# Kernel tuning notes

Measured on AMD Instinct MI355X. Metric: run time of the kernel, lower is better.

The kernel has to match this reference:

```python
import jax, jax.numpy as jnp
import numpy as np

_EPS = 1e-5
RC = 5.0   # cutoff radius
L = 20     # number of radial basis functions
N = 10000  # nodes
E = 100000 # edges
F = 128    # in_feats


def _ssp(x):
    # ShiftedSoftplus: softplus(x) - log(2)
    return jax.nn.softplus(x) - jnp.log(2.0)


def _rbf(r):
    # DimeNet radial basis: sqrt(2/rc) * sin(n*pi*r/rc) / r, n = 1..L.  r: [E,1] -> [E,L]
    n = jnp.arange(1, L + 1, dtype=r.dtype)
    return jnp.sqrt(2.0 / RC) * jnp.sin(n * jnp.pi * r / RC) / r


def _fc(u):
    # cosine cutoff applied elementwise: 0.5*(cos(pi*u/rc)+1) for u < rc else 0
    return jnp.where(u < RC, 0.5 * (jnp.cos(jnp.pi * u / RC) + 1.0), 0.0)


def setup_inputs() -> dict:
    key = jax.random.key(0)
    ks = jax.random.split(key, 12)

    def nrm(k, shape, scale=1.0):
        return jax.random.normal(k, shape, dtype=jnp.float32) * scale

    return {
        "x": nrm(ks[0], (N, 3)) * 3.0,           # atomic positions
        "v": nrm(ks[1], (N, F, 3)),               # vector node features
        "s": nrm(ks[2], (N, F)),                  # scalar node features
        "ms1_w": nrm(ks[3], (F, F), F ** -0.5),
        "ms1_b": jnp.zeros((F,), jnp.float32),
        "ms2_w": nrm(ks[4], (3 * F, F), F ** -0.5),
        "ms2_b": jnp.zeros((3 * F,), jnp.float32),
        "mv_w": nrm(ks[5], (3 * F, L), L ** -0.5),
        "mv_b": jnp.zeros((3 * F,), jnp.float32),
        "us1_w": nrm(ks[6], (F, F), F ** -0.5),
        "us1_b": jnp.zeros((F,), jnp.float32),
        "us2_w": nrm(ks[7], (3 * F, F), F ** -0.5),
        "us2_b": jnp.zeros((3 * F,), jnp.float32),
        "src": jax.random.randint(ks[8], (E,), 0, N, dtype=jnp.int32),
        "dst": jax.random.randint(ks[9], (E,), 0, N, dtype=jnp.int32),
    }


def reference(x, v, s, ms1_w, ms1_b, ms2_w, ms2_b, mv_w, mv_b,
              us1_w, us1_b, us2_w, us2_b, src, dst):
    # ---------- pass 1: message1 + reduce1 (sum over incoming edges) ----------
    sj = s[src]                                   # [E,F]   src scalar features
    vj = v[src]                                   # [E,F,3] src vector features
    vec = x[src] - x[dst]                         # [E,3]   x_i - x_j (molecule branch)
    r = jnp.sqrt(jnp.sum(vec ** 2, axis=-1) + _EPS)[:, None]          # [E,1]
    phi = _ssp(sj @ ms1_w.T + ms1_b) @ ms2_w.T + ms2_b                 # [E,3F]
    w = _fc(_rbf(r) @ mv_w.T + mv_b)                                    # [E,3F]
    v_, s_, r_ = jnp.split(phi * w, 3, axis=-1)                         # each [E,F]
    dv_e = vj * v_[:, :, None] + r_[:, :, None] * (vec / r)[:, None, :] # [E,F,3]
    dv = jax.ops.segment_sum(dv_e, dst, num_segments=N)                 # [N,F,3]
    ds = jax.ops.segment_sum(s_, dst, num_segments=N)                   # [N,F]
    v_new = v + dv
    s_new = s + ds

    # ---------- pass 2: message2 + reduce2 (mean over incoming edges) ----------
    s2 = _ssp(s_new[src] @ us1_w.T + us1_b) @ us2_w.T + us2_b           # [E,3F]
    deg = jax.ops.segment_sum(jnp.ones((E,), s.dtype), dst, num_segments=N)
    denom = jnp.maximum(deg, 1.0)
    s_mean = jax.ops.segment_sum(s2, dst, num_segments=N) / denom[:, None]        # [N,3F]
    uv = jax.ops.segment_sum(v_new[src], dst, num_segments=N) / denom[:, None, None]  # [N,F,3]
    avv, asv, ass = jnp.split(s_mean, 3, axis=-1)                       # each [N,F]
    norm = jnp.sqrt(jnp.sum(uv ** 2, axis=-1) + _EPS)[..., None]        # [N,F,1]
    dv2 = uv * avv[:, :, None]                                           # [N,F,3]
    ds2 = jnp.sum((uv / norm) ** 2, axis=-1) * asv + ass                 # [N,F]
    return (v_new + dv2, s_new + ds2)
```

## Files before the change

### kernel.cpp

```cpp
#include <hip/hip_runtime.h>
#include <hip/hip_bf16.h>


#define F_DIM   128
#define F3_DIM  384
#define L_DIM   20
#define CAP     64
#define BATCH   16

typedef __attribute__((ext_vector_type(8))) short short8;
typedef __attribute__((ext_vector_type(4))) float f32x4;
typedef __attribute__((ext_vector_type(4))) unsigned short us4;

struct u3 { unsigned a, b, c; };

__device__ __forceinline__ unsigned short f2bf(float f) {
  union { float f; unsigned u; } a; a.f = f;
  unsigned u = a.u;
  u = (u + 0x7FFFu + ((u >> 16) & 1u)) >> 16;
  return (unsigned short)u;
}
__device__ __forceinline__ float bf2f(unsigned short u) {
  union { unsigned u; float f; } a; a.u = ((unsigned)u) << 16;
  return a.f;
}

__global__ __launch_bounds__(256) void cast_fill_kernel(
    const float* __restrict__ ms1_w, unsigned short* __restrict__ w_ms1,
    const float* __restrict__ ms2_w, unsigned short* __restrict__ w_ms2,
    const float* __restrict__ us1_w, unsigned short* __restrict__ w_us1,
    const float* __restrict__ us2_w, unsigned short* __restrict__ w_us2,
    const float* __restrict__ s,     unsigned short* __restrict__ sbf,
    const float* __restrict__ v,     us4* __restrict__ v4,
    const float* __restrict__ mv_w,  unsigned short* __restrict__ mvwB,
    const int* __restrict__ src, const int* __restrict__ dst,
    int* __restrict__ cursor, int* __restrict__ jbuf,
    unsigned short* __restrict__ c1pad, unsigned short* __restrict__ v4pad,
    int nF, int E)
{
  int i = blockIdx.x * 256 + threadIdx.x;
  if (i < 16384) w_ms1[i] = f2bf(ms1_w[i]);
  if (i < 49152) w_ms2[i] = f2bf(ms2_w[i]);
  if (i < 16384) w_us1[i] = f2bf(us1_w[i]);
  if (i < 49152) w_us2[i] = f2bf(us2_w[i]);
  if (i < nF)    sbf[i] = f2bf(s[i]);
  if (i < nF) {
    const float* vp = v + (size_t)i * 3;
    us4 o; o.x = f2bf(vp[0]); o.y = f2bf(vp[1]); o.z = f2bf(vp[2]); o.w = 0;
    v4[i] = o;
  }
  if (i < 384 * 32) {
    int o = i >> 5, k = i & 31;
    float val = (k < 20) ? mv_w[o * 20 + k] * 0.6324555320336759f : 0.f;
    mvwB[i] = f2bf(val);
  }
  if (i < 768) c1pad[i] = 0;
  if (i < 512) v4pad[i] = 0;
  if (i < E) {
    int d = dst[i];
    int p = atomicAdd(&cursor[d], 1);
    if (p < CAP) jbuf[d * CAP + p] = src[i];
  }
}

__global__ __launch_bounds__(512) void mlp_kernel(
    const unsigned short* __restrict__ X,
    const unsigned short* __restrict__ W1,
    const float* __restrict__ B1,
    const unsigned short* __restrict__ W2,
    const float* __restrict__ B2,
    const us4* __restrict__ Vin,
    unsigned short* __restrict__ Yc)
{
  __shared__ float HT[128 * 17];
  const int lane = threadIdx.x & 63;
  const int wave = threadIdx.x >> 6;
  const int c    = lane & 15;
  const int quad = lane >> 4;
  const int m0   = blockIdx.x * 16;

  f32x4 acc = (f32x4){0.f, 0.f, 0.f, 0.f};
#pragma unroll
  for (int kk = 0; kk < 4; kk++) {
    short8 a = *(const short8*)(X + (size_t)(m0 + c) * 128 + kk * 32 + quad * 8);
    short8 b = *(const short8*)(W1 + (size_t)(wave * 16 + c) * 128 + kk * 32 + quad * 8);
    acc = __builtin_amdgcn_mfma_f32_16x16x32_bf16(a, b, acc, 0, 0, 0);
  }
  {
    int k = wave * 16 + c;
    float bias = B1[k];
#pragma unroll
    for (int r = 0; r < 4; r++) {
      float h = acc[r] + bias;
      float sp = (h > 15.f) ? h : log1pf(__expf(h));
      sp -= 0.69314718056f;
      HT[k * 17 + quad * 4 + r] = sp;
    }
  }
  __syncthreads();

  f32x4 acc2[3];
#pragma unroll
  for (int g = 0; g < 3; g++) acc2[g] = (f32x4){0.f, 0.f, 0.f, 0.f};
#pragma unroll
  for (int kk = 0; kk < 4; kk++) {
    short8 afr;
#pragma unroll
    for (int j = 0; j < 8; j++) {
      float hv = HT[(kk * 32 + quad * 8 + j) * 17 + c];
      afr[j] = (short)f2bf(hv);
    }
#pragma unroll
    for (int g = 0; g < 3; g++) {
      short8 b = *(const short8*)(W2 + (size_t)(g * 128 + wave * 16 + c) * 128 + kk * 32 + quad * 8);
      acc2[g] = __builtin_amdgcn_mfma_f32_16x16x32_bf16(afr, b, acc2[g], 0, 0, 0);
    }
  }
  {
    int f = wave * 16 + c;
    float b0 = B2[f], b1 = B2[128 + f], b2 = B2[256 + f];
#pragma unroll
    for (int r = 0; r < 4; r++) {
      int m = quad * 4 + r;
      us4 vv = Vin[(size_t)(m0 + m) * 128 + f];
      unsigned p0 = f2bf(acc2[0][r] + b0);
      unsigned p1 = f2bf(acc2[1][r] + b1);
      unsigned p2 = f2bf(acc2[2][r] + b2);
      u3 rec;
      rec.a = p0 | (p1 << 16);
      rec.b = p2 | ((unsigned)vv.x << 16);
      rec.c = (unsigned)vv.y | ((unsigned)vv.z << 16);
      *(u3*)(Yc + ((size_t)(m0 + m) * 128 + f) * 6) = rec;
    }
  }
}

__global__ __launch_bounds__(512) void hidden_kernel(
    const unsigned short* __restrict__ X,
    const unsigned short* __restrict__ W1,
    const float* __restrict__ B1,
    us4* __restrict__ V4)
{
  const int lane = threadIdx.x & 63;
  const int wave = threadIdx.x >> 6;
  const int c    = lane & 15;
  const int quad = lane >> 4;
  const int m0   = blockIdx.x * 16;

  f32x4 acc = (f32x4){0.f, 0.f, 0.f, 0.f};
#pragma unroll
  for (int kk = 0; kk < 4; kk++) {
    short8 a = *(const short8*)(X + (size_t)(m0 + c) * 128 + kk * 32 + quad * 8);
    short8 b = *(const short8*)(W1 + (size_t)(wave * 16 + c) * 128 + kk * 32 + quad * 8);
    acc = __builtin_amdgcn_mfma_f32_16x16x32_bf16(a, b, acc, 0, 0, 0);
  }
  int f = wave * 16 + c;
  float bias = B1[f];
#pragma unroll
  for (int r = 0; r < 4; r++) {
    int m = m0 + quad * 4 + r;
    float h = acc[r] + bias;
    float sp = (h > 15.f) ? h : log1pf(__expf(h));
    sp -= 0.69314718056f;
    us4 rec = V4[(size_t)m * 128 + f];
    rec.w = f2bf(sp);
    V4[(size_t)m * 128 + f] = rec;
  }
}

__global__ __launch_bounds__(256, 4) void pass1_kernel(
    const float* __restrict__ x,
    const unsigned short* __restrict__ combo1,
    const float* __restrict__ v,
    const float* __restrict__ s,
    const unsigned short* __restrict__ mvwB,
    const float* __restrict__ mv_b,
    const int* __restrict__ jbuf,
    const int* __restrict__ deg,
    float* __restrict__ vnew, us4* __restrict__ vnew4,
    float* __restrict__ snew, unsigned short* __restrict__ snew_bf, int nNodes)
{
  __shared__ unsigned short Asn[BATCH * 32];
  __shared__ float4 Au[BATCH];
  __shared__ us4 Wl[BATCH * 128];
  __shared__ float red[512];

  const int tid  = threadIdx.x;
  const int wave = tid >> 6, lane = tid & 63;
  const int half = wave >> 1, split = wave & 1;
  const int i = blockIdx.x;
  const int f = lane + 64 * half;
  const int c = lane & 15, quad = lane >> 4;

  int cnt = deg[i]; if (cnt > CAP) cnt = CAP;
  const int base = i * CAP;

  short8 bfr[6]; float bias[6];
#pragma unroll
  for (int p = 0; p < 3; p++)
#pragma unroll
    for (int h = 0; h < 2; h++) {
      int t = 2 * wave + h + 8 * p;
      bfr[p * 2 + h]  = *(const short8*)(mvwB + (size_t)(t * 16 + c) * 32 + quad * 8);
      bias[p * 2 + h] = mv_b[t * 16 + c];
    }

  const float xi0 = x[i * 3], xi1 = x[i * 3 + 1], xi2 = x[i * 3 + 2];
  int jv = (lane < cnt) ? jbuf[base + lane] : nNodes;

  float accV0 = 0.f, accV1 = 0.f, accV2 = 0.f, accS = 0.f;

  for (int bs = 0; bs < cnt; bs += BATCH) {
    int bcnt = cnt - bs; if (bcnt > BATCH) bcnt = BATCH;
    __syncthreads();

    if (wave == 0) {
      int t16 = lane & (BATCH - 1);
      int e = bs + t16;
      int j = __shfl(jv, e);
      if (lane < BATCH && e < cnt) {
        float d0 = x[j * 3]     - xi0;
        float d1 = x[j * 3 + 1] - xi1;
        float d2 = x[j * 3 + 2] - xi2;
        float r = sqrtf(d0 * d0 + d1 * d1 + d2 * d2 + 1e-5f);
        float invr = 1.0f / r;
        Au[lane] = make_float4(d0 * invr, d1 * invr, d2 * invr, invr);
        float theta = r * 0.6283185307179586f;
        float s1, c1;
        __sincosf(theta, &s1, &c1);
        float c2 = 2.f * c1;
        float pm2 = s1, pm1 = c2 * s1;
        Asn[lane * 32 + 0] = f2bf(pm2);
        Asn[lane * 32 + 1] = f2bf(pm1);
#pragma unroll
        for (int l = 2; l < L_DIM; l++) {
          float cur = c2 * pm1 - pm2;
          Asn[lane * 32 + l] = f2bf(cur);
          pm2 = pm1; pm1 = cur;
        }
#pragma unroll
        for (int l = L_DIM; l < 32; l++) Asn[lane * 32 + l] = 0;
      }
    }
    __syncthreads();

    {
      short8 a = *(const short8*)&Asn[c * 32 + quad * 8];
      f32x4 acc[6];
#pragma unroll
      for (int q = 0; q < 6; q++)
        acc[q] = __builtin_amdgcn_mfma_f32_16x16x32_bf16(
            a, bfr[q], (f32x4){0.f, 0.f, 0.f, 0.f}, 0, 0, 0);
#pragma unroll
      for (int r = 0; r < 4; r++) {
        int el = quad * 4 + r;
        if (el < bcnt) {
          float invr = Au[el].w;
#pragma unroll
          for (int h = 0; h < 2; h++) {
            float wp0 = fmaf(acc[h][r],     invr, bias[h]);
            float wp1 = fmaf(acc[2 + h][r], invr, bias[2 + h]);
            float wp2 = fmaf(acc[4 + h][r], invr, bias[4 + h]);
            float w0 = (wp0 < 5.f) ? 0.5f * (__cosf(wp0 * 0.6283185307179586f) + 1.f) : 0.f;
            float w1 = (wp1 < 5.f) ? 0.5f * (__cosf(wp1 * 0.6283185307179586f) + 1.f) : 0.f;
            float w2 = (wp2 < 5.f) ? 0.5f * (__cosf(wp2 * 0.6283185307179586f) + 1.f) : 0.f;
            us4 o; o.x = f2bf(w0); o.y = f2bf(w1); o.z = f2bf(w2); o.w = 0;
            Wl[el * 128 + wave * 32 + h * 16 + c] = o;
          }
        }
      }
    }
    __syncthreads();

    u3 cb[8];
#pragma unroll
    for (int k = 0; k < 8; k++) {
      int j = __shfl(jv, bs + split + 2 * k);
      cb[k] = *(const u3*)(combo1 + ((size_t)j * 128 + f) * 6);
    }
#pragma unroll
    for (int k = 0; k < 8; k++) {
      int el = split + 2 * k;
      if (el < bcnt) {
        float4 u = Au[el];
        us4 wv = Wl[el * 128 + f];
        float ph0 = bf2f((unsigned short)(cb[k].a & 0xffff));
        float ph1 = bf2f((unsigned short)(cb[k].a >> 16));
        float ph2 = bf2f((unsigned short)(cb[k].b & 0xffff));
        float vx  = bf2f((unsigned short)(cb[k].b >> 16));
        float vy  = bf2f((unsigned short)(cb[k].c & 0xffff));
        float vz  = bf2f((unsigned short)(cb[k].c >> 16));
        float m0 = ph0 * bf2f(wv.x);
        float m1 = ph1 * bf2f(wv.y);
        float m2 = ph2 * bf2f(wv.z);
        accV0 = fmaf(vx, m0, fmaf(m2, u.x, accV0));
        accV1 = fmaf(vy, m0, fmaf(m2, u.y, accV1));
        accV2 = fmaf(vz, m0, fmaf(m2, u.z, accV2));
        accS += m1;
      }
    }
  }

  const int idx = half * 64 + lane;
  __syncthreads();
  if (split == 1) {
    red[idx * 4 + 0] = accV0; red[idx * 4 + 1] = accV1;
    red[idx * 4 + 2] = accV2; red[idx * 4 + 3] = accS;
  }
  __syncthreads();
  if (split == 0) {
    accV0 += red[idx * 4 + 0]; accV1 += red[idx * 4 + 1];
    accV2 += red[idx * 4 + 2]; accS  += red[idx * 4 + 3];
    size_t b3 = (size_t)i * 384 + f * 3;
    float n0 = v[b3] + accV0, n1 = v[b3 + 1] + accV1, n2 = v[b3 + 2] + accV2;
    vnew[b3] = n0; vnew[b3 + 1] = n1; vnew[b3 + 2] = n2;
    us4 o; o.x = f2bf(n0); o.y = f2bf(n1); o.z = f2bf(n2); o.w = 0;
    vnew4[(size_t)i * 128 + f] = o;
    size_t b1 = (size_t)i * 128 + f;
    float sv = s[b1] + accS;
    snew[b1] = sv;
    snew_bf[b1] = f2bf(sv);
  }
}

__global__ __launch_bounds__(512, 2) void pass2_kernel(
    const us4* __restrict__ vnew4,
    const int* __restrict__ jbuf, const int* __restrict__ deg,
    const unsigned short* __restrict__ W2,
    const float* __restrict__ B2,
    const float* __restrict__ vnew,
    const float* __restrict__ snew,
    float* __restrict__ vout, float* __restrict__ sout, int nNodes)
{
  __shared__ unsigned short HMb[16][136];
  __shared__ float UV[16 * 128 * 3];

  const int tid  = threadIdx.x;
  const int wave = tid >> 6, lane = tid & 63;
  const int c    = lane & 15, quad = lane >> 4;
  const int m0   = blockIdx.x * 16;

  const int ra = 2 * wave, rb = ra + 1;
  const int na = m0 + ra, nb = m0 + rb;
  int ca = deg[na]; if (ca > CAP) ca = CAP;
  int cb = deg[nb]; if (cb > CAP) cb = CAP;
  int jva = (lane < ca) ? jbuf[na * CAP + lane] : nNodes;
  int jvb = (lane < cb) ? jbuf[nb * CAP + lane] : nNodes;

  float a0l = 0.f, a1l = 0.f, a2l = 0.f, ahl = 0.f;
  float a0h = 0.f, a1h = 0.f, a2h = 0.f, ahh = 0.f;
  float b0l = 0.f, b1l = 0.f, b2l = 0.f, bhl = 0.f;
  float b0h = 0.f, b1h = 0.f, b2h = 0.f, bhh = 0.f;

  int emax = (ca > cb) ? ca : cb;
  for (int e = 0; e < emax; ++e) {
    int ja = __shfl(jva, e);
    int jb = __shfl(jvb, e);
    us4 ral = vnew4[(size_t)ja * 128 + lane];
    us4 rah = vnew4[(size_t)ja * 128 + lane + 64];
    us4 rbl = vnew4[(size_t)jb * 128 + lane];
    us4 rbh = vnew4[(size_t)jb * 128 + lane + 64];
    a0l += bf2f(ral.x); a1l += bf2f(ral.y); a2l += bf2f(ral.z); ahl += bf2f(ral.w);
    a0h += bf2f(rah.x); a1h += bf2f(rah.y); a2h += bf2f(rah.z); ahh += bf2f(rah.w);
    b0l += bf2f(rbl.x); b1l += bf2f(rbl.y); b2l += bf2f(rbl.z); bhl += bf2f(rbl.w);
    b0h += bf2f(rbh.x); b1h += bf2f(rbh.y); b2h += bf2f(rbh.z); bhh += bf2f(rbh.w);
  }

  float dia = 1.0f / (float)(ca > 0 ? ca : 1);
  float dib = 1.0f / (float)(cb > 0 ? cb : 1);
  {
    int fl = lane, fh = lane + 64;
    UV[(ra * 128 + fl) * 3 + 0] = a0l * dia;
    UV[(ra * 128 + fl) * 3 + 1] = a1l * dia;
    UV[(ra * 128 + fl) * 3 + 2] = a2l * dia;
    UV[(ra * 128 + fh) * 3 + 0] = a0h * dia;
    UV[(ra * 128 + fh) * 3 + 1] = a1h * dia;
    UV[(ra * 128 + fh) * 3 + 2] = a2h * dia;
    UV[(rb * 128 + fl) * 3 + 0] = b0l * dib;
    UV[(rb * 128 + fl) * 3 + 1] = b1l * dib;
    UV[(rb * 128 + fl) * 3 + 2] = b2l * dib;
    UV[(rb * 128 + fh) * 3 + 0] = b0h * dib;
    UV[(rb * 128 + fh) * 3 + 1] = b1h * dib;
    UV[(rb * 128 + fh) * 3 + 2] = b2h * dib;
    HMb[ra][fl] = f2bf(ahl * dia);
    HMb[ra][fh] = f2bf(ahh * dia);
    HMb[rb][fl] = f2bf(bhl * dib);
    HMb[rb][fh] = f2bf(bhh * dib);
  }
  __syncthreads();

  f32x4 acc2[3];
#pragma unroll
  for (int g = 0; g < 3; g++) acc2[g] = (f32x4){0.f, 0.f, 0.f, 0.f};
#pragma unroll
  for (int kk = 0; kk < 4; kk++) {
    short8 afr = *(const short8*)&HMb[c][kk * 32 + quad * 8];
#pragma unroll
    for (int g = 0; g < 3; g++) {
      short8 b = *(const short8*)(W2 + (size_t)(g * 128 + wave * 16 + c) * 128 + kk * 32 + quad * 8);
      acc2[g] = __builtin_amdgcn_mfma_f32_16x16x32_bf16(afr, b, acc2[g], 0, 0, 0);
    }
  }

  int f = wave * 16 + c;
  float bb0 = B2[f], bb1 = B2[128 + f], bb2 = B2[256 + f];
#pragma unroll
  for (int r = 0; r < 4; r++) {
    int m = quad * 4 + r;
    int gm = m0 + m;
    float z = (deg[gm] > 0) ? 1.f : 0.f;
    float avv = (acc2[0][r] + bb0) * z;
    float asv = (acc2[1][r] + bb1) * z;
    float ass = (acc2[2][r] + bb2) * z;
    float uv0 = UV[(m * 128 + f) * 3 + 0];
    float uv1 = UV[(m * 128 + f) * 3 + 1];
    float uv2 = UV[(m * 128 + f) * 3 + 2];
    float q = uv0 * uv0 + uv1 * uv1 + uv2 * uv2;
    float ds2 = (q / (q + 1e-5f)) * asv + ass;
    size_t b3 = (size_t)gm * 384 + f * 3;
    vout[b3]     = vnew[b3]     + uv0 * avv;
    vout[b3 + 1] = vnew[b3 + 1] + uv1 * avv;
    vout[b3 + 2] = vnew[b3 + 2] + uv2 * avv;
    size_t b1i = (size_t)gm * 128 + f;
    sout[b1i] = snew[b1i] + ds2;
  }
}

extern "C" void kernel_launch(void* const* d_in, const int* in_sizes, int n_in,
                              void* d_out, int out_size, void* d_ws, size_t ws_size,
                              hipStream_t stream)
{
  const float* x     = (const float*)d_in[0];
  const float* v     = (const float*)d_in[1];
  const float* s     = (const float*)d_in[2];
  const float* ms1_w = (const float*)d_in[3];
  const float* ms1_b = (const float*)d_in[4];
  const float* ms2_w = (const float*)d_in[5];
  const float* ms2_b = (const float*)d_in[6];
  const float* mv_w  = (const float*)d_in[7];
  const float* mv_b  = (const float*)d_in[8];
  const float* us1_w = (const float*)d_in[9];
  const float* us1_b = (const float*)d_in[10];
  const float* us2_w = (const float*)d_in[11];
  const float* us2_b = (const float*)d_in[12];
  const int*   src   = (const int*)d_in[13];
  const int*   dst   = (const int*)d_in[14];

  const int N = in_sizes[0] / 3;
  const int E = in_sizes[13];

  char* p = (char*)d_ws;
  auto alloc = [&](size_t bytes) -> void* {
    void* r = (void*)p;
    p += (bytes + 255) & ~(size_t)255;
    return r;
  };
  unsigned short* sbf   = (unsigned short*)alloc((size_t)N * 128 * 2);
  unsigned short* snbf  = (unsigned short*)alloc((size_t)N * 128 * 2);
  unsigned short* w_ms1 = (unsigned short*)alloc(16384 * 2);
  unsigned short* w_ms2 = (unsigned short*)alloc(49152 * 2);
  unsigned short* w_us1 = (unsigned short*)alloc(16384 * 2);
  unsigned short* w_us2 = (unsigned short*)alloc(49152 * 2);
  unsigned short* mvwB  = (unsigned short*)alloc(384 * 32 * 2);
  us4*   v4     = (us4*)alloc((size_t)N * 128 * 8);
  us4*   vnew4  = (us4*)alloc((size_t)(N + 1) * 128 * 8);
  unsigned short* combo1 = (unsigned short*)alloc((size_t)(N + 1) * 128 * 12);
  float* vnew   = (float*)alloc((size_t)N * 384 * 4);
  float* snew   = (float*)alloc((size_t)N * 128 * 4);
  int* cursor   = (int*)alloc((size_t)N * 4);
  int* jbuf     = (int*)alloc((size_t)N * CAP * 4);

  hipMemsetAsync(cursor, 0, (size_t)N * 4, stream);

  cast_fill_kernel<<<(N * 128 + 255) / 256, 256, 0, stream>>>(
      ms1_w, w_ms1, ms2_w, w_ms2, us1_w, w_us1, us2_w, w_us2,
      s, sbf, v, v4, mv_w, mvwB, src, dst, cursor, jbuf,
      combo1 + (size_t)N * 768, (unsigned short*)(vnew4 + (size_t)N * 128),
      N * 128, E);

  mlp_kernel<<<N / 16, 512, 0, stream>>>(sbf, w_ms1, ms1_b, w_ms2, ms2_b,
                                         v4, combo1);

  pass1_kernel<<<N, 256, 0, stream>>>(x, combo1, v, s, mvwB, mv_b,
                                      jbuf, cursor, vnew, vnew4, snew, snbf, N);

  hidden_kernel<<<N / 16, 512, 0, stream>>>(snbf, w_us1, us1_b, vnew4);

  float* vout = (float*)d_out;
  float* sout = vout + (size_t)N * 384;
  pass2_kernel<<<N / 16, 512, 0, stream>>>(vnew4, jbuf, cursor, w_us2, us2_b,
                                           vnew, snew, vout, sout, N);
}
```

Baseline: 213.3 us.

## Fuse v bf16 cast into MLP, parallelize RBF setup, unroll pass2 gather

The bf16 conversion of v moves out of cast_fill_kernel into the MLP epilogue, which now reads fp32 v directly, so the intermediate v4 buffer and its write and re-read are gone. In pass1 the radial-basis setup is spread across all threads (16 threads per edge), each computing sin(n*theta) directly instead of one wave running a serial Chebyshev recurrence per edge. The pass2 gather loop is unrolled by two edges to keep more loads in flight. The costs are more transcendental calls per edge and a strided fp32 read of v in the MLP epilogue.

```diff
diff --git a/kernel.cpp b/kernel.cpp
--- a/kernel.cpp
+++ b/kernel.cpp
@@ -31,7 +31,6 @@
     const float* __restrict__ us1_w, unsigned short* __restrict__ w_us1,
     const float* __restrict__ us2_w, unsigned short* __restrict__ w_us2,
     const float* __restrict__ s,     unsigned short* __restrict__ sbf,
-    const float* __restrict__ v,     us4* __restrict__ v4,
     const float* __restrict__ mv_w,  unsigned short* __restrict__ mvwB,
     const int* __restrict__ src, const int* __restrict__ dst,
     int* __restrict__ cursor, int* __restrict__ jbuf,
@@ -44,11 +43,6 @@
   if (i < 16384) w_us1[i] = f2bf(us1_w[i]);
   if (i < 49152) w_us2[i] = f2bf(us2_w[i]);
   if (i < nF)    sbf[i] = f2bf(s[i]);
-  if (i < nF) {
-    const float* vp = v + (size_t)i * 3;
-    us4 o; o.x = f2bf(vp[0]); o.y = f2bf(vp[1]); o.z = f2bf(vp[2]); o.w = 0;
-    v4[i] = o;
-  }
   if (i < 384 * 32) {
     int o = i >> 5, k = i & 31;
     float val = (k < 20) ? mv_w[o * 20 + k] * 0.6324555320336759f : 0.f;
@@ -69,7 +63,7 @@
     const float* __restrict__ B1,
     const unsigned short* __restrict__ W2,
     const float* __restrict__ B2,
-    const us4* __restrict__ Vin,
+    const float* __restrict__ Vfp,
     unsigned short* __restrict__ Yc)
 {
   __shared__ float HT[128 * 17];
@@ -122,14 +116,14 @@
 #pragma unroll
     for (int r = 0; r < 4; r++) {
       int m = quad * 4 + r;
-      us4 vv = Vin[(size_t)(m0 + m) * 128 + f];
+      const float* vp = Vfp + ((size_t)(m0 + m) * 128 + f) * 3;
       unsigned p0 = f2bf(acc2[0][r] + b0);
       unsigned p1 = f2bf(acc2[1][r] + b1);
       unsigned p2 = f2bf(acc2[2][r] + b2);
       u3 rec;
       rec.a = p0 | (p1 << 16);
-      rec.b = p2 | ((unsigned)vv.x << 16);
-      rec.c = (unsigned)vv.y | ((unsigned)vv.z << 16);
+      rec.b = p2 | ((unsigned)f2bf(vp[0]) << 16);
+      rec.c = (unsigned)f2bf(vp[1]) | ((unsigned)f2bf(vp[2]) << 16);
       *(u3*)(Yc + ((size_t)(m0 + m) * 128 + f) * 6) = rec;
     }
   }
@@ -214,32 +208,22 @@
     int bcnt = cnt - bs; if (bcnt > BATCH) bcnt = BATCH;
     __syncthreads();
 
-    if (wave == 0) {
-      int t16 = lane & (BATCH - 1);
-      int e = bs + t16;
-      int j = __shfl(jv, e);
-      if (lane < BATCH && e < cnt) {
+    {
+      int e  = tid >> 4;
+      int li = tid & 15;
+      int j  = __shfl(jv, bs + e);
+      if (e < bcnt) {
         float d0 = x[j * 3]     - xi0;
         float d1 = x[j * 3 + 1] - xi1;
         float d2 = x[j * 3 + 2] - xi2;
         float r = sqrtf(d0 * d0 + d1 * d1 + d2 * d2 + 1e-5f);
         float invr = 1.0f / r;
-        Au[lane] = make_float4(d0 * invr, d1 * invr, d2 * invr, invr);
+        if (li == 0) Au[e] = make_float4(d0 * invr, d1 * invr, d2 * invr, invr);
         float theta = r * 0.6283185307179586f;
-        float s1, c1;
-        __sincosf(theta, &s1, &c1);
-        float c2 = 2.f * c1;
-        float pm2 = s1, pm1 = c2 * s1;
-        Asn[lane * 32 + 0] = f2bf(pm2);
-        Asn[lane * 32 + 1] = f2bf(pm1);
-#pragma unroll
-        for (int l = 2; l < L_DIM; l++) {
-          float cur = c2 * pm1 - pm2;
-          Asn[lane * 32 + l] = f2bf(cur);
-          pm2 = pm1; pm1 = cur;
-        }
-#pragma unroll
-        for (int l = L_DIM; l < 32; l++) Asn[lane * 32 + l] = 0;
+        Asn[e * 32 + li] = f2bf(__sinf((float)(li + 1) * theta));
+        unsigned short hiv = 0;
+        if (li < 4) hiv = f2bf(__sinf((float)(li + 17) * theta));
+        Asn[e * 32 + 16 + li] = hiv;
       }
     }
     __syncthreads();
@@ -353,17 +337,27 @@
   float b0h = 0.f, b1h = 0.f, b2h = 0.f, bhh = 0.f;
 
   int emax = (ca > cb) ? ca : cb;
-  for (int e = 0; e < emax; ++e) {
-    int ja = __shfl(jva, e);
-    int jb = __shfl(jvb, e);
-    us4 ral = vnew4[(size_t)ja * 128 + lane];
-    us4 rah = vnew4[(size_t)ja * 128 + lane + 64];
-    us4 rbl = vnew4[(size_t)jb * 128 + lane];
-    us4 rbh = vnew4[(size_t)jb * 128 + lane + 64];
-    a0l += bf2f(ral.x); a1l += bf2f(ral.y); a2l += bf2f(ral.z); ahl += bf2f(ral.w);
-    a0h += bf2f(rah.x); a1h += bf2f(rah.y); a2h += bf2f(rah.z); ahh += bf2f(rah.w);
-    b0l += bf2f(rbl.x); b1l += bf2f(rbl.y); b2l += bf2f(rbl.z); bhl += bf2f(rbl.w);
-    b0h += bf2f(rbh.x); b1h += bf2f(rbh.y); b2h += bf2f(rbh.z); bhh += bf2f(rbh.w);
+  for (int e = 0; e < emax; e += 2) {
+    int ja0 = __shfl(jva, e);
+    int jb0 = __shfl(jvb, e);
+    int ja1 = __shfl(jva, e + 1);
+    int jb1 = __shfl(jvb, e + 1);
+    us4 r0al = vnew4[(size_t)ja0 * 128 + lane];
+    us4 r0ah = vnew4[(size_t)ja0 * 128 + lane + 64];
+    us4 r0bl = vnew4[(size_t)jb0 * 128 + lane];
+    us4 r0bh = vnew4[(size_t)jb0 * 128 + lane + 64];
+    us4 r1al = vnew4[(size_t)ja1 * 128 + lane];
+    us4 r1ah = vnew4[(size_t)ja1 * 128 + lane + 64];
+    us4 r1bl = vnew4[(size_t)jb1 * 128 + lane];
+    us4 r1bh = vnew4[(size_t)jb1 * 128 + lane + 64];
+    a0l += bf2f(r0al.x) + bf2f(r1al.x); a1l += bf2f(r0al.y) + bf2f(r1al.y);
+    a2l += bf2f(r0al.z) + bf2f(r1al.z); ahl += bf2f(r0al.w) + bf2f(r1al.w);
+    a0h += bf2f(r0ah.x) + bf2f(r1ah.x); a1h += bf2f(r0ah.y) + bf2f(r1ah.y);
+    a2h += bf2f(r0ah.z) + bf2f(r1ah.z); ahh += bf2f(r0ah.w) + bf2f(r1ah.w);
+    b0l += bf2f(r0bl.x) + bf2f(r1bl.x); b1l += bf2f(r0bl.y) + bf2f(r1bl.y);
+    b2l += bf2f(r0bl.z) + bf2f(r1bl.z); bhl += bf2f(r0bl.w) + bf2f(r1bl.w);
+    b0h += bf2f(r0bh.x) + bf2f(r1bh.x); b1h += bf2f(r0bh.y) + bf2f(r1bh.y);
+    b2h += bf2f(r0bh.z) + bf2f(r1bh.z); bhh += bf2f(r0bh.w) + bf2f(r1bh.w);
   }
 
   float dia = 1.0f / (float)(ca > 0 ? ca : 1);
@@ -462,7 +456,6 @@
   unsigned short* w_us1 = (unsigned short*)alloc(16384 * 2);
   unsigned short* w_us2 = (unsigned short*)alloc(49152 * 2);
   unsigned short* mvwB  = (unsigned short*)alloc(384 * 32 * 2);
-  us4*   v4     = (us4*)alloc((size_t)N * 128 * 8);
   us4*   vnew4  = (us4*)alloc((size_t)(N + 1) * 128 * 8);
   unsigned short* combo1 = (unsigned short*)alloc((size_t)(N + 1) * 128 * 12);
   float* vnew   = (float*)alloc((size_t)N * 384 * 4);
@@ -474,12 +467,12 @@
 
   cast_fill_kernel<<<(N * 128 + 255) / 256, 256, 0, stream>>>(
       ms1_w, w_ms1, ms2_w, w_ms2, us1_w, w_us1, us2_w, w_us2,
-      s, sbf, v, v4, mv_w, mvwB, src, dst, cursor, jbuf,
+      s, sbf, mv_w, mvwB, src, dst, cursor, jbuf,
       combo1 + (size_t)N * 768, (unsigned short*)(vnew4 + (size_t)N * 128),
       N * 128, E);
 
   mlp_kernel<<<N / 16, 512, 0, stream>>>(sbf, w_ms1, ms1_b, w_ms2, ms2_b,
-                                         v4, combo1);
+                                         v, combo1);
 
   pass1_kernel<<<N, 256, 0, stream>>>(x, combo1, v, s, mvwB, mv_b,
                                       jbuf, cursor, vnew, vnew4, snew, snbf, N);
```

Measured after the change: 209.7 us. Within noise of the previous version (-1.7%).
